# Kernel tuning notes

Hardware: AMD Instinct MI355X
Metric: run time of the kernel (lower is better)

The kernel has to match this reference:

```python
import jax, jax.numpy as jnp
import numpy as np

EMBED_DIM = 1024
NUM_HEADS = 16
HEAD_DIM = EMBED_DIM // NUM_HEADS
B, S = 4, 2048


def setup_inputs() -> dict:
    key = jax.random.key(0)
    ks = jax.random.split(key, 12)
    s = 1.0 / np.sqrt(EMBED_DIM)
    inp = {
        'q': jax.random.normal(ks[0], (B, S, EMBED_DIM), jnp.float32),
        'k': jax.random.normal(ks[1], (B, S, EMBED_DIM), jnp.float32),
        'v': jax.random.normal(ks[2], (B, S, EMBED_DIM), jnp.float32),
        'mask': jnp.tril(jnp.ones((S, S), jnp.int32))[None, None],  # [1,1,S,S] causal
        'Wq': jax.random.normal(ks[3], (EMBED_DIM, EMBED_DIM), jnp.float32) * s,
        'bq': jax.random.normal(ks[4], (EMBED_DIM,), jnp.float32) * s,
        'Wk': jax.random.normal(ks[5], (EMBED_DIM, EMBED_DIM), jnp.float32) * s,
        'bk': jax.random.normal(ks[6], (EMBED_DIM,), jnp.float32) * s,
        'Wv': jax.random.normal(ks[7], (EMBED_DIM, EMBED_DIM), jnp.float32) * s,
        'bv': jax.random.normal(ks[8], (EMBED_DIM,), jnp.float32) * s,
        'Wo': jax.random.normal(ks[9], (EMBED_DIM, EMBED_DIM), jnp.float32) * s,
        'bo': jax.random.normal(ks[10], (EMBED_DIM,), jnp.float32) * s,
    }
    return inp


def _split(x):
    b, s, _ = x.shape
    return x.reshape(b, s, NUM_HEADS, HEAD_DIM).transpose(0, 2, 1, 3)  # [b,h,s,d]


def reference(q, k, v, mask, Wq, bq, Wk, bk, Wv, bv, Wo, bo):
    # torch Linear: x @ W.T + b
    Q = _split(q @ Wq.T + bq)
    K = _split(k @ Wk.T + bk)
    V = _split(v @ Wv.T + bv)
    scores = jnp.einsum('bhqd,bhkd->bhqk', Q, K) / np.sqrt(HEAD_DIM).astype(np.float32)
    scores = jnp.where(mask == 0, jnp.float32(-1e9), scores)
    attn = jax.nn.softmax(scores, axis=-1)  # dropout p=0.0 -> identity
    out = jnp.einsum('bhqk,bhkd->bhqd', attn, V)
    out = out.transpose(0, 2, 1, 3).reshape(q.shape[0], q.shape[1], EMBED_DIM)
    return out @ Wo.T + bo
```

## Files before the change

kernel.cpp:

```cpp
#include <hip/hip_runtime.h>

#define SEQ   2048
#define EMB   1024
#define NH    16
#define HD    64
#define BATCH 4

typedef __attribute__((ext_vector_type(8))) short short8;
typedef __attribute__((ext_vector_type(4))) float floatx4;
typedef __attribute__((ext_vector_type(4))) uint uintx4;

static __device__ __forceinline__ ushort f2bf_rne(float x) {
  unsigned u = __float_as_uint(x);
  unsigned r = u + 0x7FFFu + ((u >> 16) & 1u);
  return (ushort)(r >> 16);
}
static __device__ __forceinline__ float bf2f(ushort h) {
  return __uint_as_float(((unsigned)h) << 16);
}

static __device__ __forceinline__ uint pk_bf16(float a, float b) {
  uint r;
  asm("v_cvt_pk_bf16_f32 %0, %1, %2" : "=v"(r) : "v"(a), "v"(b));
  return r;
}
static __device__ __forceinline__ void split_pair(float a, float b, uint& h,
                                                  uint& l) {
  h = pk_bf16(a, b);
  const float ha = __uint_as_float(h << 16);
  const float hb = __uint_as_float(h & 0xFFFF0000u);
  l = pk_bf16(a - ha, b - hb);
}

static __device__ __forceinline__ void load16(const void* g, void* l) {
  __builtin_amdgcn_global_load_lds(
      (const __attribute__((address_space(1))) unsigned int*)g,
      (__attribute__((address_space(3))) unsigned int*)l, 16, 0, 0);
}

static __device__ __forceinline__ int swz_off(int row, int kg) {
  return (row >> 1) * 128 + (((row & 1) << 2) + (kg ^ ((row >> 1) & 3))) * 16;
}

static __device__ __forceinline__ void stage_tile(const ushort* __restrict__ g,
                                                  int row0, int k0,
                                                  ushort* lds, int t) {
#pragma unroll
  for (int i = 0; i < 2; ++i) {
    const int slot = t + i * 256;
    const int line = slot >> 3, s = slot & 7;
    const int row = line * 2 + (s >> 2);
    const int c = (s & 3) ^ (line & 3);
    load16(g + (size_t)(row0 + row) * EMB + k0 + c * 8, lds + slot * 8);
  }
}

__global__ __launch_bounds__(256) void wconv_kernel(const float* __restrict__ W,
                                                    ushort* __restrict__ Yh,
                                                    ushort* __restrict__ Yl) {
  const int i = (blockIdx.x * 256 + threadIdx.x) * 8;
  const float4 a = *(const float4*)(W + i);
  const float4 b = *(const float4*)(W + i + 4);
  const float xv[8] = {a.x, a.y, a.z, a.w, b.x, b.y, b.z, b.w};
  uintx4 H, L;
#pragma unroll
  for (int j = 0; j < 4; ++j) {
    uint h, l;
    split_pair(xv[2 * j], xv[2 * j + 1], h, l);
    H[j] = h;
    L[j] = l;
  }
  *(uintx4*)&Yh[i] = H;
  *(uintx4*)&Yl[i] = L;
}

template <int MODE, bool PREA, bool PREB>
__global__ __launch_bounds__(256) void proj_mfma_kernel(
    const float* __restrict__ X, const ushort* __restrict__ Xh,
    const ushort* __restrict__ Xl, const float* __restrict__ W,
    const ushort* __restrict__ Wh, const ushort* __restrict__ Wl,
    const float* __restrict__ bias, float* __restrict__ Yf,
    ushort* __restrict__ Yh, ushort* __restrict__ Yl) {
  constexpr bool DBUF = (PREA || PREB);
  constexpr int NB = DBUF ? 2 : 1;
  constexpr int ASZ = PREA ? 128 * 32 : 128 * 40;
  constexpr int BSZ = PREB ? 128 * 32 : 128 * 40;
  __shared__ ushort Ahi[NB][ASZ], Alo[NB][ASZ];
  __shared__ ushort Bhi[NB][BSZ], Blo[NB][BSZ];

  const int t = threadIdx.x;
  const int lane = t & 63, wave = t >> 6;
  const int m0 = blockIdx.y * 128, n0 = blockIdx.x * 128;
  const int wm = (wave >> 1) * 64, wn = (wave & 1) * 64;
  const int fr = lane & 15, kg = lane >> 4;

  floatx4 acc[4][4];
#pragma unroll
  for (int i = 0; i < 4; ++i)
#pragma unroll
    for (int j = 0; j < 4; ++j)
#pragma unroll
      for (int r = 0; r < 4; ++r) acc[i][j][r] = 0.f;

  auto stageB = [&](int k0, int b) {
    if constexpr (PREB) {
      stage_tile(Wh, n0, k0, Bhi[b], t);
      stage_tile(Wl, n0, k0, Blo[b], t);
    } else {
#pragma unroll
      for (int i = 0; i < 4; ++i) {
        const int f = t + 256 * i;
        const int row = f >> 3, kq = f & 7;
        const float4 v =
            *(const float4*)(W + (size_t)(n0 + row) * EMB + k0 + kq * 4);
        uint h0, l0, h1, l1;
        split_pair(v.x, v.y, h0, l0);
        split_pair(v.z, v.w, h1, l1);
        uint2 hp, lp;
        hp.x = h0; hp.y = h1;
        lp.x = l0; lp.y = l1;
        *(uint2*)&Bhi[b][row * 40 + kq * 4] = hp;
        *(uint2*)&Blo[b][row * 40 + kq * 4] = lp;
      }
    }
  };
  auto stageA = [&](int k0, int b) {
    if constexpr (PREA) {
      stage_tile(Xh, m0, k0, Ahi[b], t);
      stage_tile(Xl, m0, k0, Alo[b], t);
    } else {
#pragma unroll
      for (int i = 0; i < 4; ++i) {
        const int f = t + 256 * i;
        const int row = f >> 3, kq = f & 7;
        const float4 v =
            *(const float4*)(X + (size_t)(m0 + row) * EMB + k0 + kq * 4);
        uint h0, l0, h1, l1;
        split_pair(v.x, v.y, h0, l0);
        split_pair(v.z, v.w, h1, l1);
        uint2 hp, lp;
        hp.x = h0; hp.y = h1;
        lp.x = l0; lp.y = l1;
        *(uint2*)&Ahi[b][row * 40 + kq * 4] = hp;
        *(uint2*)&Alo[b][row * 40 + kq * 4] = lp;
      }
    }
  };
  auto computeStep = [&](int cur) {
    short8 bhv[4], blv[4];
#pragma unroll
    for (int nf = 0; nf < 4; ++nf) {
      const int row = wn + nf * 16 + fr;
      if constexpr (PREB) {
        const int off = swz_off(row, kg);
        bhv[nf] = *(const short8*)((const char*)Bhi[cur] + off);
        blv[nf] = *(const short8*)((const char*)Blo[cur] + off);
      } else {
        bhv[nf] = *(const short8*)&Bhi[cur][row * 40 + kg * 8];
        blv[nf] = *(const short8*)&Blo[cur][row * 40 + kg * 8];
      }
    }
#pragma unroll
    for (int mf = 0; mf < 4; ++mf) {
      const int arow = wm + mf * 16 + fr;
      short8 ah, al;
      if constexpr (PREA) {
        const int off = swz_off(arow, kg);
        ah = *(const short8*)((const char*)Ahi[cur] + off);
        al = *(const short8*)((const char*)Alo[cur] + off);
      } else {
        ah = *(const short8*)&Ahi[cur][arow * 40 + kg * 8];
        al = *(const short8*)&Alo[cur][arow * 40 + kg * 8];
      }
#pragma unroll
      for (int nf = 0; nf < 4; ++nf) {
        acc[mf][nf] = __builtin_amdgcn_mfma_f32_16x16x32_bf16(ah, bhv[nf],
                                                              acc[mf][nf], 0, 0, 0);
        acc[mf][nf] = __builtin_amdgcn_mfma_f32_16x16x32_bf16(ah, blv[nf],
                                                              acc[mf][nf], 0, 0, 0);
        acc[mf][nf] = __builtin_amdgcn_mfma_f32_16x16x32_bf16(al, bhv[nf],
                                                              acc[mf][nf], 0, 0, 0);
      }
    }
  };

  if constexpr (DBUF) {
    stageB(0, 0);
    stageA(0, 0);
    asm volatile("s_waitcnt vmcnt(0)");
    __syncthreads();
#pragma unroll 1
    for (int k0 = 0; k0 < EMB; k0 += 32) {
      const int cur = (k0 >> 5) & 1;
      if (k0 + 32 < EMB) {
        stageB(k0 + 32, cur ^ 1);
        stageA(k0 + 32, cur ^ 1);
      }
      computeStep(cur);
      asm volatile("s_waitcnt vmcnt(0)");
      __syncthreads();
    }
  } else {
#pragma unroll 1
    for (int k0 = 0; k0 < EMB; k0 += 32) {
      __syncthreads();
      stageB(k0, 0);
      stageA(k0, 0);
      __syncthreads();
      computeStep(0);
    }
  }

  const int rg = lane >> 4;
#pragma unroll
  for (int nf = 0; nf < 4; ++nf) {
    const int n = n0 + wn + nf * 16 + fr;
    const float bb = bias[n];
    if (MODE == 2) {
      const int hh = n >> 6, d = n & 63;
#pragma unroll
      for (int mf = 0; mf < 4; ++mf) {
        const int mb = m0 + wm + mf * 16 + rg * 4;
        const int b = mb >> 11, s = mb & (SEQ - 1);
        uint h0, l0, h1, l1;
        split_pair(acc[mf][nf][0] + bb, acc[mf][nf][1] + bb, h0, l0);
        split_pair(acc[mf][nf][2] + bb, acc[mf][nf][3] + bb, h1, l1);
        uint2 hp, lp;
        hp.x = h0; hp.y = h1;
        lp.x = l0; lp.y = l1;
        const int idx = (b * NH + hh) * (HD * SEQ) + d * SEQ + s;
        *(uint2*)&Yh[idx] = hp;
        *(uint2*)&Yl[idx] = lp;
      }
    } else {
#pragma unroll
      for (int mf = 0; mf < 4; ++mf) {
#pragma unroll
        for (int r = 0; r < 4; ++r) {
          const int m = m0 + wm + mf * 16 + rg * 4 + r;
          float val = acc[mf][nf][r] + bb;
          if (MODE == 3) {
            Yf[(size_t)m * EMB + n] = val;
          } else {
            if (MODE == 0) val *= 0.125f;
            const int hh = n >> 6, d = n & 63;
            const int b = m >> 11, s = m & (SEQ - 1);
            const int idx = ((b * NH + hh) * SEQ + s) * HD + d;
            const ushort h = f2bf_rne(val);
            Yh[idx] = h;
            Yl[idx] = f2bf_rne(val - bf2f(h));
          }
        }
      }
    }
  }
}

template <bool SPLITOUT>
__global__ __launch_bounds__(256, 2) void attn_mfma_kernel(
    const ushort* __restrict__ Qh, const ushort* __restrict__ Ql,
    const ushort* __restrict__ Kh, const ushort* __restrict__ Kl,
    const ushort* __restrict__ Vth, const ushort* __restrict__ Vtl,
    float* __restrict__ O, ushort* __restrict__ Oh, ushort* __restrict__ Ol) {
  __shared__ __align__(16) ushort KHs[2][64 * 64], KLs[2][64 * 64];
  __shared__ __align__(16) ushort VHs[2][64 * 64], VLs[2][64 * 64];

  const int bh = blockIdx.x;
  const int qtA = blockIdx.y;
  const int qtB = 15 - qtA;
  const int t = threadIdx.x;
  const int lane = t & 63, wave = t >> 6;
  const int fr = lane & 15, kg = lane >> 4;
  const int base = bh * (SEQ * HD);
  const int r8 = lane >> 3, c8 = lane & 7;

  const int q00[2] = {qtA * 128 + wave * 32, qtB * 128 + wave * 32};
  const int ext[2] = {(q00[0] + 95) >> 6, (q00[1] + 95) >> 6};
  const int nkt = 2 * qtB + 2;

  short8 qfh[2][2][2], qfl[2][2][2];
#pragma unroll
  for (int g = 0; g < 2; ++g)
#pragma unroll
    for (int mf = 0; mf < 2; ++mf)
#pragma unroll
      for (int ks = 0; ks < 2; ++ks) {
        const int idx = base + (q00[g] + mf * 16 + fr) * HD + ks * 32 + kg * 8;
        qfh[g][mf][ks] = *(const short8*)&Qh[idx];
        qfl[g][mf][ks] = *(const short8*)&Ql[idx];
      }

  floatx4 oacc[2][2][4];
  float m_run[2][2], l_run[2][2];
#pragma unroll
  for (int g = 0; g < 2; ++g)
#pragma unroll
    for (int mf = 0; mf < 2; ++mf) {
#pragma unroll
      for (int nf = 0; nf < 4; ++nf)
#pragma unroll
        for (int r = 0; r < 4; ++r) oacc[g][mf][nf][r] = 0.f;
      m_run[g][mf] = -INFINITY;
      l_run[g][mf] = 0.f;
    }

  auto stage = [&](int kt, int b) {
#pragma unroll
    for (int i = 0; i < 2; ++i) {
      const int lrow = wave * 16 + i * 8;
      const int row = lrow + r8;
      const int sw = (c8 ^ (row & 7)) << 3;
      const int gk = base + (kt * 64 + row) * HD + sw;
      const int gv = base + row * SEQ + kt * 64 + sw;
      load16(Kh + gk, (char*)KHs + b * 8192 + lrow * 128);
      load16(Kl + gk, (char*)KLs + b * 8192 + lrow * 128);
      load16(Vth + gv, (char*)VHs + b * 8192 + lrow * 128);
      load16(Vtl + gv, (char*)VLs + b * 8192 + lrow * 128);
    }
  };

  stage(0, 0);
  asm volatile("s_waitcnt vmcnt(0)");
  __syncthreads();

#pragma unroll 1
  for (int kt = 0; kt < nkt; ++kt) {
    const int cur = kt & 1;
    if (kt + 1 < nkt) stage(kt + 1, cur ^ 1);
    const int c0 = kt * 64;
    const int kb = cur * 8192;

#pragma unroll
    for (int g = 0; g < 2; ++g) {
      if (kt < ext[g]) {
        const int q0 = q00[g];

        floatx4 s2[2][4];
#pragma unroll
        for (int mf = 0; mf < 2; ++mf)
#pragma unroll
          for (int nf = 0; nf < 4; ++nf)
#pragma unroll
            for (int r = 0; r < 4; ++r) s2[mf][nf][r] = 0.f;

        __builtin_amdgcn_s_setprio(1);
#pragma unroll
        for (int ksd = 0; ksd < 2; ++ksd)
#pragma unroll
          for (int nf = 0; nf < 4; ++nf) {
            const int kr =
                32 * (nf >> 1) + 8 * (fr >> 2) + 4 * (nf & 1) + (fr & 3);
            const int byo = kb + kr * 128 + (((ksd * 4 + kg) ^ (kr & 7)) << 4);
            const short8 kh = *(const short8*)((const char*)KHs + byo);
            const short8 kl = *(const short8*)((const char*)KLs + byo);
#pragma unroll
            for (int mf = 0; mf < 2; ++mf) {
              s2[mf][nf] = __builtin_amdgcn_mfma_f32_16x16x32_bf16(
                  kh, qfh[g][mf][ksd], s2[mf][nf], 0, 0, 0);
              s2[mf][nf] = __builtin_amdgcn_mfma_f32_16x16x32_bf16(
                  kh, qfl[g][mf][ksd], s2[mf][nf], 0, 0, 0);
              s2[mf][nf] = __builtin_amdgcn_mfma_f32_16x16x32_bf16(
                  kl, qfh[g][mf][ksd], s2[mf][nf], 0, 0, 0);
            }
          }
        __builtin_amdgcn_s_setprio(0);

        if (c0 + 63 > q0) {
#pragma unroll
          for (int mf = 0; mf < 2; ++mf)
#pragma unroll
            for (int nf = 0; nf < 4; ++nf)
#pragma unroll
              for (int r = 0; r < 4; ++r) {
                const int col =
                    c0 + 32 * (nf >> 1) + 8 * kg + 4 * (nf & 1) + r;
                const int row = q0 + mf * 16 + fr;
                if (col > row) s2[mf][nf][r] = -1e9f;
              }
        }

        float pmv[2];
#pragma unroll
        for (int mf = 0; mf < 2; ++mf) {
          float pm = s2[mf][0][0];
#pragma unroll
          for (int nf = 0; nf < 4; ++nf)
#pragma unroll
            for (int r = 0; r < 4; ++r) pm = fmaxf(pm, s2[mf][nf][r]);
          pm = fmaxf(pm, __shfl_xor(pm, 16));
          pm = fmaxf(pm, __shfl_xor(pm, 32));
          pmv[mf] = pm;
        }
        float alpha2[2] = {1.f, 1.f};
        const bool grow = !__all((pmv[0] <= m_run[g][0] + 8.f) &&
                                 (pmv[1] <= m_run[g][1] + 8.f));
        if (grow) {
#pragma unroll
          for (int mf = 0; mf < 2; ++mf) {
            const float mnew = fmaxf(m_run[g][mf], pmv[mf]);
            alpha2[mf] = __expf(m_run[g][mf] - mnew);
            m_run[g][mf] = mnew;
          }
#pragma unroll
          for (int mf = 0; mf < 2; ++mf)
#pragma unroll
            for (int r = 0; r < 4; ++r) {
              const float a = __shfl(alpha2[mf], (kg * 4 + r) | (lane & 48));
#pragma unroll
              for (int nf = 0; nf < 4; ++nf) oacc[g][mf][nf][r] *= a;
            }
        }
#pragma unroll
        for (int mf = 0; mf < 2; ++mf) {
          const float mm = m_run[g][mf];
          float sum = 0.f;
#pragma unroll
          for (int nf = 0; nf < 4; ++nf)
#pragma unroll
            for (int r = 0; r < 4; ++r) {
              const float p = __expf(s2[mf][nf][r] - mm);
              s2[mf][nf][r] = p;
              sum += p;
            }
          sum += __shfl_xor(sum, 16);
          sum += __shfl_xor(sum, 32);
          l_run[g][mf] = l_run[g][mf] * alpha2[mf] + sum;
        }

        short8 pah[2][2], pal[2][2];
#pragma unroll
        for (int mf = 0; mf < 2; ++mf)
#pragma unroll
          for (int ks = 0; ks < 2; ++ks) {
            uintx4 H, L;
#pragma unroll
            for (int jj = 0; jj < 4; ++jj) {
              const int nfi = 2 * ks + (jj >> 1);
              uint h, l;
              split_pair(s2[mf][nfi][(2 * jj) & 3], s2[mf][nfi][(2 * jj + 1) & 3],
                         h, l);
              H[jj] = h;
              L[jj] = l;
            }
            pah[mf][ks] = *(short8*)&H;
            pal[mf][ks] = *(short8*)&L;
          }

        __builtin_amdgcn_s_setprio(1);
#pragma unroll
        for (int ks = 0; ks < 2; ++ks)
#pragma unroll
          for (int nf = 0; nf < 4; ++nf) {
            const int d = nf * 16 + fr;
            const int byo = kb + d * 128 + (((ks * 4 + kg) ^ (d & 7)) << 4);
            const short8 vh = *(const short8*)((const char*)VHs + byo);
            const short8 vl = *(const short8*)((const char*)VLs + byo);
#pragma unroll
            for (int mf = 0; mf < 2; ++mf) {
              oacc[g][mf][nf] = __builtin_amdgcn_mfma_f32_16x16x32_bf16(
                  pah[mf][ks], vh, oacc[g][mf][nf], 0, 0, 0);
              oacc[g][mf][nf] = __builtin_amdgcn_mfma_f32_16x16x32_bf16(
                  pah[mf][ks], vl, oacc[g][mf][nf], 0, 0, 0);
              oacc[g][mf][nf] = __builtin_amdgcn_mfma_f32_16x16x32_bf16(
                  pal[mf][ks], vh, oacc[g][mf][nf], 0, 0, 0);
            }
          }
        __builtin_amdgcn_s_setprio(0);
      }
    }

    asm volatile("s_waitcnt vmcnt(0)");
    __syncthreads();
  }

  const int b = bh >> 4, hsel = bh & 15;
#pragma unroll
  for (int g = 0; g < 2; ++g)
#pragma unroll
    for (int mf = 0; mf < 2; ++mf)
#pragma unroll
      for (int r = 0; r < 4; ++r) {
        const float lv = __shfl(l_run[g][mf], (kg * 4 + r) | (lane & 48));
        const float inv = 1.f / lv;
        const int grow2 = q00[g] + mf * 16 + kg * 4 + r;
        const int rowbase = (b * SEQ + grow2) * EMB + hsel * HD;
#pragma unroll
        for (int nf = 0; nf < 4; ++nf) {
          const float val = oacc[g][mf][nf][r] * inv;
          const int idx = rowbase + nf * 16 + fr;
          if constexpr (SPLITOUT) {
            const ushort hh = f2bf_rne(val);
            Oh[idx] = hh;
            Ol[idx] = f2bf_rne(val - bf2f(hh));
          } else {
            O[idx] = val;
          }
        }
      }
}

extern "C" void kernel_launch(void* const* d_in, const int* in_sizes, int n_in,
                              void* d_out, int out_size, void* d_ws,
                              size_t ws_size, hipStream_t stream) {
  const float* q = (const float*)d_in[0];
  const float* k = (const float*)d_in[1];
  const float* v = (const float*)d_in[2];
  const float* Wq = (const float*)d_in[4];
  const float* bq = (const float*)d_in[5];
  const float* Wk = (const float*)d_in[6];
  const float* bk = (const float*)d_in[7];
  const float* Wv = (const float*)d_in[8];
  const float* bv = (const float*)d_in[9];
  const float* Wo = (const float*)d_in[10];
  const float* bo = (const float*)d_in[11];
  float* out = (float*)d_out;

  const size_t E = (size_t)BATCH * SEQ * EMB;
  const size_t WE = (size_t)EMB * EMB;
  ushort* us = (ushort*)d_ws;
  ushort* Qh = us;
  ushort* Ql = us + E;
  ushort* Kh = us + 2 * E;
  ushort* Kl = us + 3 * E;
  ushort* Vth = us + 4 * E;
  ushort* Vtl = us + 5 * E;

  const dim3 pgrid(EMB / 128, (BATCH * SEQ) / 128);
  const dim3 agrid(BATCH * NH, 8);
  const dim3 blk(256);
  const int wgrid = (int)(WE / 8 / 256);

  if (ws_size >= 8 * E * sizeof(ushort)) {
    ushort* W3 = us + 6 * E;
    ushort* Wqh = W3, *Wql = W3 + WE;
    ushort* Wkh = W3 + 2 * WE, *Wkl = W3 + 3 * WE;
    ushort* Wvh = W3 + 4 * WE, *Wvl = W3 + 5 * WE;
    ushort* AOh = us + 6 * E, *AOl = us + 7 * E;
    ushort* Woh = us, *Wol = us + WE;

    wconv_kernel<<<wgrid, blk, 0, stream>>>(Wq, Wqh, Wql);
    wconv_kernel<<<wgrid, blk, 0, stream>>>(Wk, Wkh, Wkl);
    wconv_kernel<<<wgrid, blk, 0, stream>>>(Wv, Wvh, Wvl);
    proj_mfma_kernel<0, false, true><<<pgrid, blk, 0, stream>>>(
        q, nullptr, nullptr, nullptr, Wqh, Wql, bq, nullptr, Qh, Ql);
    proj_mfma_kernel<1, false, true><<<pgrid, blk, 0, stream>>>(
        k, nullptr, nullptr, nullptr, Wkh, Wkl, bk, nullptr, Kh, Kl);
    proj_mfma_kernel<2, false, true><<<pgrid, blk, 0, stream>>>(
        v, nullptr, nullptr, nullptr, Wvh, Wvl, bv, nullptr, Vth, Vtl);
    attn_mfma_kernel<true><<<agrid, blk, 0, stream>>>(Qh, Ql, Kh, Kl, Vth, Vtl,
                                                      nullptr, AOh, AOl);
    wconv_kernel<<<wgrid, blk, 0, stream>>>(Wo, Woh, Wol);
    proj_mfma_kernel<3, true, true><<<pgrid, blk, 0, stream>>>(
        nullptr, AOh, AOl, nullptr, Woh, Wol, bo, out, nullptr, nullptr);
  } else if (ws_size >= (6 * E + 6 * WE) * sizeof(ushort)) {
    ushort* W3 = us + 6 * E;
    ushort* Wqh = W3, *Wql = W3 + WE;
    ushort* Wkh = W3 + 2 * WE, *Wkl = W3 + 3 * WE;
    ushort* Wvh = W3 + 4 * WE, *Wvl = W3 + 5 * WE;
    ushort* AOh = (ushort*)d_out, *AOl = AOh + E;
    ushort* Woh = us, *Wol = us + WE;
    float* PO = (float*)(us + 2 * E);

    wconv_kernel<<<wgrid, blk, 0, stream>>>(Wq, Wqh, Wql);
    wconv_kernel<<<wgrid, blk, 0, stream>>>(Wk, Wkh, Wkl);
    wconv_kernel<<<wgrid, blk, 0, stream>>>(Wv, Wvh, Wvl);
    proj_mfma_kernel<0, false, true><<<pgrid, blk, 0, stream>>>(
        q, nullptr, nullptr, nullptr, Wqh, Wql, bq, nullptr, Qh, Ql);
    proj_mfma_kernel<1, false, true><<<pgrid, blk, 0, stream>>>(
        k, nullptr, nullptr, nullptr, Wkh, Wkl, bk, nullptr, Kh, Kl);
    proj_mfma_kernel<2, false, true><<<pgrid, blk, 0, stream>>>(
        v, nullptr, nullptr, nullptr, Wvh, Wvl, bv, nullptr, Vth, Vtl);
    attn_mfma_kernel<true><<<agrid, blk, 0, stream>>>(Qh, Ql, Kh, Kl, Vth, Vtl,
                                                      nullptr, AOh, AOl);
    wconv_kernel<<<wgrid, blk, 0, stream>>>(Wo, Woh, Wol);
    proj_mfma_kernel<3, true, true><<<pgrid, blk, 0, stream>>>(
        nullptr, AOh, AOl, nullptr, Woh, Wol, bo, PO, nullptr, nullptr);
    hipError_t e1 = hipMemcpyAsync(out, PO, E * sizeof(float),
                                   hipMemcpyDeviceToDevice, stream);
    (void)e1;
  } else {
    float* AO = out;
    float* PO = (float*)d_ws;
    proj_mfma_kernel<0, false, false><<<pgrid, blk, 0, stream>>>(
        q, nullptr, nullptr, Wq, nullptr, nullptr, bq, nullptr, Qh, Ql);
    proj_mfma_kernel<1, false, false><<<pgrid, blk, 0, stream>>>(
        k, nullptr, nullptr, Wk, nullptr, nullptr, bk, nullptr, Kh, Kl);
    proj_mfma_kernel<2, false, false><<<pgrid, blk, 0, stream>>>(
        v, nullptr, nullptr, Wv, nullptr, nullptr, bv, nullptr, Vth, Vtl);
    attn_mfma_kernel<false><<<agrid, blk, 0, stream>>>(
        Qh, Ql, Kh, Kl, Vth, Vtl, AO, nullptr, nullptr);
    proj_mfma_kernel<3, false, false><<<pgrid, blk, 0, stream>>>(
        AO, nullptr, nullptr, Wo, nullptr, nullptr, bo, PO, nullptr, nullptr);
    hipError_t e2 = hipMemcpyAsync(out, PO, E * sizeof(float),
                                   hipMemcpyDeviceToDevice, stream);
    (void)e2;
  }
}
```

Baseline: 369.9 us.

## Prefetch fp32 A tiles into registers, merge weight conversions, drop setprio

```diff
diff --git a/kernel.cpp b/kernel.cpp
--- a/kernel.cpp
+++ b/kernel.cpp
@@ -53,6 +53,33 @@
     const int c = (s & 3) ^ (line & 3);
     load16(g + (size_t)(row0 + row) * EMB + k0 + c * 8, lds + slot * 8);
   }
+}
+
+__global__ __launch_bounds__(256) void wconv3_kernel(
+    const float* __restrict__ Wq, const float* __restrict__ Wk,
+    const float* __restrict__ Wv, ushort* __restrict__ Yqh,
+    ushort* __restrict__ Yql, ushort* __restrict__ Ykh,
+    ushort* __restrict__ Ykl, ushort* __restrict__ Yvh,
+    ushort* __restrict__ Yvl) {
+  const int which = blockIdx.x >> 9;
+  const int bid = blockIdx.x & 511;
+  const float* W = which == 0 ? Wq : which == 1 ? Wk : Wv;
+  ushort* Yh = which == 0 ? Yqh : which == 1 ? Ykh : Yvh;
+  ushort* Yl = which == 0 ? Yql : which == 1 ? Ykl : Yvl;
+  const int i = (bid * 256 + threadIdx.x) * 8;
+  const float4 a = *(const float4*)(W + i);
+  const float4 b = *(const float4*)(W + i + 4);
+  const float xv[8] = {a.x, a.y, a.z, a.w, b.x, b.y, b.z, b.w};
+  uintx4 H, L;
+#pragma unroll
+  for (int j = 0; j < 4; ++j) {
+    uint h, l;
+    split_pair(xv[2 * j], xv[2 * j + 1], h, l);
+    H[j] = h;
+    L[j] = l;
+  }
+  *(uintx4*)&Yh[i] = H;
+  *(uintx4*)&Yl[i] = L;
 }
 
 __global__ __launch_bounds__(256) void wconv_kernel(const float* __restrict__ W,
@@ -124,26 +151,33 @@
       }
     }
   };
-  auto stageA = [&](int k0, int b) {
+  auto loadA_regs = [&](int k0, float4* xr) {
+#pragma unroll
+    for (int i = 0; i < 4; ++i) {
+      const int f = t + 256 * i;
+      const int row = f >> 3, kq = f & 7;
+      xr[i] = *(const float4*)(X + (size_t)(m0 + row) * EMB + k0 + kq * 4);
+    }
+  };
+  auto writeA_regs = [&](const float4* xr, int b) {
+#pragma unroll
+    for (int i = 0; i < 4; ++i) {
+      const int f = t + 256 * i;
+      const int row = f >> 3, kq = f & 7;
+      uint h0, l0, h1, l1;
+      split_pair(xr[i].x, xr[i].y, h0, l0);
+      split_pair(xr[i].z, xr[i].w, h1, l1);
+      uint2 hp, lp;
+      hp.x = h0; hp.y = h1;
+      lp.x = l0; lp.y = l1;
+      *(uint2*)&Ahi[b][row * 40 + kq * 4] = hp;
+      *(uint2*)&Alo[b][row * 40 + kq * 4] = lp;
+    }
+  };
+  auto stageA_pre = [&](int k0, int b) {
     if constexpr (PREA) {
       stage_tile(Xh, m0, k0, Ahi[b], t);
       stage_tile(Xl, m0, k0, Alo[b], t);
-    } else {
-#pragma unroll
-      for (int i = 0; i < 4; ++i) {
-        const int f = t + 256 * i;
-        const int row = f >> 3, kq = f & 7;
-        const float4 v =
-            *(const float4*)(X + (size_t)(m0 + row) * EMB + k0 + kq * 4);
-        uint h0, l0, h1, l1;
-        split_pair(v.x, v.y, h0, l0);
-        split_pair(v.z, v.w, h1, l1);
-        uint2 hp, lp;
-        hp.x = h0; hp.y = h1;
-        lp.x = l0; lp.y = l1;
-        *(uint2*)&Ahi[b][row * 40 + kq * 4] = hp;
-        *(uint2*)&Alo[b][row * 40 + kq * 4] = lp;
-      }
     }
   };
   auto computeStep = [&](int cur) {
@@ -184,9 +218,9 @@
     }
   };
 
-  if constexpr (DBUF) {
+  if constexpr (PREA && PREB) {
     stageB(0, 0);
-    stageA(0, 0);
+    stageA_pre(0, 0);
     asm volatile("s_waitcnt vmcnt(0)");
     __syncthreads();
 #pragma unroll 1
@@ -194,9 +228,32 @@
       const int cur = (k0 >> 5) & 1;
       if (k0 + 32 < EMB) {
         stageB(k0 + 32, cur ^ 1);
-        stageA(k0 + 32, cur ^ 1);
+        stageA_pre(k0 + 32, cur ^ 1);
       }
       computeStep(cur);
+      asm volatile("s_waitcnt vmcnt(0)");
+      __syncthreads();
+    }
+  } else if constexpr (PREB) {
+    stageB(0, 0);
+    {
+      float4 xr0[4];
+      loadA_regs(0, xr0);
+      writeA_regs(xr0, 0);
+    }
+    asm volatile("s_waitcnt vmcnt(0)");
+    __syncthreads();
+#pragma unroll 1
+    for (int k0 = 0; k0 < EMB; k0 += 32) {
+      const int cur = (k0 >> 5) & 1;
+      const bool more = (k0 + 32 < EMB);
+      float4 xr[4];
+      if (more) {
+        loadA_regs(k0 + 32, xr);
+        stageB(k0 + 32, cur ^ 1);
+      }
+      computeStep(cur);
+      if (more) writeA_regs(xr, cur ^ 1);
       asm volatile("s_waitcnt vmcnt(0)");
       __syncthreads();
     }
@@ -205,7 +262,11 @@
     for (int k0 = 0; k0 < EMB; k0 += 32) {
       __syncthreads();
       stageB(k0, 0);
-      stageA(k0, 0);
+      {
+        float4 xr0[4];
+        loadA_regs(k0, xr0);
+        writeA_regs(xr0, 0);
+      }
       __syncthreads();
       computeStep(0);
     }
@@ -343,7 +404,6 @@
 #pragma unroll
             for (int r = 0; r < 4; ++r) s2[mf][nf][r] = 0.f;
 
-        __builtin_amdgcn_s_setprio(1);
 #pragma unroll
         for (int ksd = 0; ksd < 2; ++ksd)
 #pragma unroll
@@ -363,7 +423,6 @@
                   kl, qfh[g][mf][ksd], s2[mf][nf], 0, 0, 0);
             }
           }
-        __builtin_amdgcn_s_setprio(0);
 
         if (c0 + 63 > q0) {
 #pragma unroll
@@ -446,7 +505,6 @@
             pal[mf][ks] = *(short8*)&L;
           }
 
-        __builtin_amdgcn_s_setprio(1);
 #pragma unroll
         for (int ks = 0; ks < 2; ++ks)
 #pragma unroll
@@ -465,7 +523,6 @@
                   pal[mf][ks], vh, oacc[g][mf][nf], 0, 0, 0);
             }
           }
-        __builtin_amdgcn_s_setprio(0);
       }
     }
 
@@ -538,9 +595,8 @@
     ushort* AOh = us + 6 * E, *AOl = us + 7 * E;
     ushort* Woh = us, *Wol = us + WE;
 
-    wconv_kernel<<<wgrid, blk, 0, stream>>>(Wq, Wqh, Wql);
-    wconv_kernel<<<wgrid, blk, 0, stream>>>(Wk, Wkh, Wkl);
-    wconv_kernel<<<wgrid, blk, 0, stream>>>(Wv, Wvh, Wvl);
+    wconv3_kernel<<<3 * wgrid, blk, 0, stream>>>(Wq, Wk, Wv, Wqh, Wql, Wkh,
+                                                 Wkl, Wvh, Wvl);
     proj_mfma_kernel<0, false, true><<<pgrid, blk, 0, stream>>>(
         q, nullptr, nullptr, nullptr, Wqh, Wql, bq, nullptr, Qh, Ql);
     proj_mfma_kernel<1, false, true><<<pgrid, blk, 0, stream>>>(
@@ -561,9 +617,8 @@
     ushort* Woh = us, *Wol = us + WE;
     float* PO = (float*)(us + 2 * E);
 
-    wconv_kernel<<<wgrid, blk, 0, stream>>>(Wq, Wqh, Wql);
-    wconv_kernel<<<wgrid, blk, 0, stream>>>(Wk, Wkh, Wkl);
-    wconv_kernel<<<wgrid, blk, 0, stream>>>(Wv, Wvh, Wvl);
+    wconv3_kernel<<<3 * wgrid, blk, 0, stream>>>(Wq, Wk, Wv, Wqh, Wql, Wkh,
+                                                 Wkl, Wvh, Wvl);
     proj_mfma_kernel<0, false, true><<<pgrid, blk, 0, stream>>>(
         q, nullptr, nullptr, nullptr, Wqh, Wql, bq, nullptr, Qh, Ql);
     proj_mfma_kernel<1, false, true><<<pgrid, blk, 0, stream>>>(
```

After: 393.9 us. 1.06x slower.
